# Kernel tuning notes

Measured on AMD Instinct MI355X. Metric: run time of the kernel, lower is better.

## Reference

```python
import jax, jax.numpy as jnp
import numpy as np

N_NODES = 100000


def _gcn_layer(x, src, dst, W, b, n_nodes):
    # x: [N, Cin]; src/dst already include self-loops
    h = x @ W  # [N, Cout]
    deg = jax.ops.segment_sum(jnp.ones_like(dst, dtype=h.dtype), dst,
                              num_segments=n_nodes)  # in-degree incl. self-loop
    dinv = jnp.where(deg > 0, deg ** -0.5, 0.0)
    norm = dinv[src] * dinv[dst]  # [E]
    msg = h[src] * norm[:, None]  # [E, Cout]
    out = jax.ops.segment_sum(msg, dst, num_segments=n_nodes)
    return out + b


def setup_inputs() -> dict:
    key = jax.random.key(0)
    k1, k2, k3, k4, k5, k6, k7 = jax.random.split(key, 7)
    E = 6400000
    x = jax.random.normal(k1, (N_NODES, 5), dtype=jnp.float32)
    edge_index = jax.random.randint(k2, (2, E), 0, N_NODES, dtype=jnp.int64)
    edge_f = jax.random.normal(k3, (E,), dtype=jnp.float32)
    edge_attr = jax.random.normal(k4, (E, 1), dtype=jnp.float32)
    # GCNConv params (glorot-ish scale)
    W1 = jax.random.normal(k5, (5, 8), dtype=jnp.float32) * (1.0 / np.sqrt(5))
    b1 = jnp.zeros((8,), dtype=jnp.float32)
    W2 = jax.random.normal(k6, (8, 5), dtype=jnp.float32) * (1.0 / np.sqrt(8))
    b2 = jnp.zeros((5,), dtype=jnp.float32)
    return {"x": x, "edge_index": edge_index, "edge_f": edge_f,
            "edge_attr": edge_attr, "W1": W1, "b1": b1, "W2": W2, "b2": b2}


def reference(x, edge_index, edge_f, edge_attr, W1, b1, W2, b2):
    n = x.shape[0]
    loops = jnp.arange(n, dtype=edge_index.dtype)
    src = jnp.concatenate([edge_index[0], loops])  # add self-loops (PyG default)
    dst = jnp.concatenate([edge_index[1], loops])
    h = _gcn_layer(x, src, dst, W1, b1, n)
    h = _gcn_layer(h, src, dst, W2, b2, n)
    return h
```

## Files before the change

kernel.cpp:

```cpp
#include <hip/hip_runtime.h>
#include <hip/hip_fp16.h>


#define TPB 256
#define VPB 256
#define B_BITS 8
#define MAXB 512
#define CAP 17408
#define NBLK_E 512
#define EPB 12500
#define SCT 512
#define DGT 512

typedef int int4e __attribute__((ext_vector_type(4)));
typedef _Float16 h8 __attribute__((ext_vector_type(8)));

__device__ __forceinline__ int4e ntload4(const int* p) {
    return __builtin_nontemporal_load((const int4e*)p);
}
__device__ __forceinline__ int ntload(const int* p) {
    return __builtin_nontemporal_load(p);
}

__global__ void k_init(int B, int* __restrict__ bpos) {
    int b = blockIdx.x * blockDim.x + threadIdx.x;
    if (b < B) bpos[b] = b * CAP;
}

__global__ __launch_bounds__(SCT) void k_scat(const int* __restrict__ src,
        const int* __restrict__ dst, int E, int B,
        int* __restrict__ bpos, int* __restrict__ pairs) {
    __shared__ int sorted[EPB];
    __shared__ int hist[MAXB], scn[MAXB], cur[MAXB], gbase[MAXB];
    int t = threadIdx.x;
    for (int i = t; i < MAXB; i += SCT) hist[i] = 0;
    __syncthreads();
    int lo = blockIdx.x * EPB;
    int n = min(E - lo, EPB);
    int n4 = n & ~3;
    for (int i = t * 4; i < n4; i += SCT * 4) {
        int4e d4 = ntload4(dst + lo + i);
        atomicAdd(&hist[d4.x >> B_BITS], 1);
        atomicAdd(&hist[d4.y >> B_BITS], 1);
        atomicAdd(&hist[d4.z >> B_BITS], 1);
        atomicAdd(&hist[d4.w >> B_BITS], 1);
    }
    for (int i = n4 + t; i < n; i += SCT)
        atomicAdd(&hist[dst[lo + i] >> B_BITS], 1);
    __syncthreads();
    if (t < MAXB) scn[t] = hist[t];
    __syncthreads();
    for (int off = 1; off < MAXB; off <<= 1) {
        int v = (t >= off && t < MAXB) ? scn[t - off] : 0;
        __syncthreads();
        if (t < MAXB) scn[t] += v;
        __syncthreads();
    }
    if (t < MAXB) {
        int h = hist[t];
        cur[t] = scn[t] - h;
        gbase[t] = (t < B && h) ? atomicAdd(&bpos[t], h) : 0;
    }
    __syncthreads();
    for (int i = t * 4; i < n4; i += SCT * 4) {
        int4e d4 = ntload4(dst + lo + i);
        int4e s4 = ntload4(src + lo + i);
        int p;
        p = atomicAdd(&cur[d4.x >> B_BITS], 1); sorted[p] = (s4.x << B_BITS) | (d4.x & (VPB - 1));
        p = atomicAdd(&cur[d4.y >> B_BITS], 1); sorted[p] = (s4.y << B_BITS) | (d4.y & (VPB - 1));
        p = atomicAdd(&cur[d4.z >> B_BITS], 1); sorted[p] = (s4.z << B_BITS) | (d4.z & (VPB - 1));
        p = atomicAdd(&cur[d4.w >> B_BITS], 1); sorted[p] = (s4.w << B_BITS) | (d4.w & (VPB - 1));
    }
    for (int i = n4 + t; i < n; i += SCT) {
        int d = dst[lo + i], s = src[lo + i];
        int p = atomicAdd(&cur[d >> B_BITS], 1);
        sorted[p] = (s << B_BITS) | (d & (VPB - 1));
    }
    __syncthreads();
    int wave = t >> 6, lane = t & 63;
    for (int b2 = wave; b2 < B; b2 += (SCT >> 6)) {
        int h = hist[b2];
        int st = scn[b2] - h;
        int gb = gbase[b2];
        for (int j = lane; j < h; j += 64)
            pairs[gb + j] = sorted[st + j];
    }
}

__global__ __launch_bounds__(DGT) void k_degxs(const int* __restrict__ pairs,
        const int* __restrict__ bpos, int N,
        const float* __restrict__ x,
        unsigned int* __restrict__ jinfo, _Float16* __restrict__ xs) {
    __shared__ int hist[VPB];
    __shared__ int scn[VPB];
    int t = threadIdx.x, b = blockIdx.x;
    if (t < VPB) hist[t] = 0;
    __syncthreads();
    int base = b * CAP;
    int n = bpos[b] - base, n4 = n & ~3;
    for (int i = t * 4; i < n4; i += DGT * 4) {
        int4e p = ntload4(pairs + base + i);
        atomicAdd(&hist[p.x & (VPB - 1)], 1);
        atomicAdd(&hist[p.y & (VPB - 1)], 1);
        atomicAdd(&hist[p.z & (VPB - 1)], 1);
        atomicAdd(&hist[p.w & (VPB - 1)], 1);
    }
    for (int i = n4 + t; i < n; i += DGT)
        atomicAdd(&hist[pairs[base + i] & (VPB - 1)], 1);
    __syncthreads();
    if (t < VPB) scn[t] = hist[t];
    __syncthreads();
    for (int off = 1; off < VPB; off <<= 1) {
        int v = (t >= off && t < VPB) ? scn[t - off] : 0;
        __syncthreads();
        if (t < VPB) scn[t] += v;
        __syncthreads();
    }
    int node = b * VPB + t;
    if (t < VPB && node < N) {
        int h = hist[t];
        int start = base + scn[t] - h;
        jinfo[node] = ((unsigned int)start << 9) | (unsigned int)h;
        float di = rsqrtf((float)(h + 1));
        const float* xp = x + (size_t)node * 5;
        h8 v;
        v[0] = (_Float16)(xp[0] * di); v[1] = (_Float16)(xp[1] * di);
        v[2] = (_Float16)(xp[2] * di); v[3] = (_Float16)(xp[3] * di);
        v[4] = (_Float16)(xp[4] * di);
        v[5] = (_Float16)0.f; v[6] = (_Float16)0.f; v[7] = (_Float16)0.f;
        *(h8*)(xs + (size_t)node * 8) = v;
    }
}

__global__ __launch_bounds__(1024) void k_agg1(const int* __restrict__ pairs_,
        const int* __restrict__ bpos, const unsigned int* __restrict__ jinfo,
        const _Float16* __restrict__ xs, const float* __restrict__ b1,
        const float* __restrict__ W1, const float* __restrict__ W2,
        _Float16* __restrict__ h2s, int N) {
    __shared__ int csr[CAP];
    __shared__ int js[VPB], ct[VPB], cur[VPB];
    int* pairs = (int*)pairs_;
    int t = threadIdx.x, b = blockIdx.x;
    int base = b * CAP;
    if (t < VPB) {
        int node = b * VPB + t;
        int s = 0, c = 0;
        if (node < N) {
            unsigned int u = jinfo[node];
            s = (int)(u >> 9) - base;
            c = (int)(u & 511u);
        }
        js[t] = s; ct[t] = c; cur[t] = s;
    }
    __syncthreads();
    int n = bpos[b] - base, n4 = n & ~3;
    for (int i = t * 4; i < n4; i += 1024 * 4) {
        int4e p = ntload4(pairs + base + i);
        int q;
        q = atomicAdd(&cur[p.x & (VPB - 1)], 1); csr[q] = p.x >> B_BITS;
        q = atomicAdd(&cur[p.y & (VPB - 1)], 1); csr[q] = p.y >> B_BITS;
        q = atomicAdd(&cur[p.z & (VPB - 1)], 1); csr[q] = p.z >> B_BITS;
        q = atomicAdd(&cur[p.w & (VPB - 1)], 1); csr[q] = p.w >> B_BITS;
    }
    for (int i = n4 + t; i < n; i += 1024) {
        int p = pairs[base + i];
        int q = atomicAdd(&cur[p & (VPB - 1)], 1);
        csr[q] = p >> B_BITS;
    }
    __syncthreads();
    for (int i = t; i < n; i += 1024)
        __builtin_nontemporal_store(csr[i], pairs + base + i);
    int lane = t & 3, ln = t >> 2;
    int node = b * VPB + ln;
    if (node >= N) return;
    int s0 = js[ln], cn = ct[ln];
    float a0 = 0.f, a1 = 0.f, a2 = 0.f, a3 = 0.f, a4 = 0.f;
    int j = lane;
    for (; j + 12 < cn; j += 16) {
        int sA = csr[s0 + j];
        int sB = csr[s0 + j + 4];
        int sC = csr[s0 + j + 8];
        int sD = csr[s0 + j + 12];
        h8 vA = *(const h8*)(xs + (size_t)sA * 8);
        h8 vB = *(const h8*)(xs + (size_t)sB * 8);
        h8 vC = *(const h8*)(xs + (size_t)sC * 8);
        h8 vD = *(const h8*)(xs + (size_t)sD * 8);
        a0 += (float)vA[0] + (float)vB[0] + (float)vC[0] + (float)vD[0];
        a1 += (float)vA[1] + (float)vB[1] + (float)vC[1] + (float)vD[1];
        a2 += (float)vA[2] + (float)vB[2] + (float)vC[2] + (float)vD[2];
        a3 += (float)vA[3] + (float)vB[3] + (float)vC[3] + (float)vD[3];
        a4 += (float)vA[4] + (float)vB[4] + (float)vC[4] + (float)vD[4];
    }
    for (; j < cn; j += 4) {
        int sA = csr[s0 + j];
        h8 vA = *(const h8*)(xs + (size_t)sA * 8);
        a0 += (float)vA[0]; a1 += (float)vA[1]; a2 += (float)vA[2];
        a3 += (float)vA[3]; a4 += (float)vA[4];
    }
#pragma unroll
    for (int d = 1; d < 4; d <<= 1) {
        a0 += __shfl_xor(a0, d); a1 += __shfl_xor(a1, d);
        a2 += __shfl_xor(a2, d); a3 += __shfl_xor(a3, d);
        a4 += __shfl_xor(a4, d);
    }
    h8 sv = *(const h8*)(xs + (size_t)node * 8);
    float tc[5];
    tc[0] = a0 + (float)sv[0]; tc[1] = a1 + (float)sv[1];
    tc[2] = a2 + (float)sv[2]; tc[3] = a3 + (float)sv[3];
    tc[4] = a4 + (float)sv[4];
    float di = rsqrtf((float)(cn + 1));
    float o1[8];
#pragma unroll
    for (int jj = 0; jj < 8; ++jj) {
        float h = 0.f;
#pragma unroll
        for (int c = 0; c < 5; ++c) h += tc[c] * W1[c * 8 + jj];
        o1[jj] = h * di + b1[jj];
    }
    if (lane == 0) {
        float hv[5];
#pragma unroll
        for (int k = 0; k < 5; ++k) {
            float h = 0.f;
#pragma unroll
            for (int jj = 0; jj < 8; ++jj) h += o1[jj] * W2[jj * 5 + k];
            hv[k] = h * di;
        }
        h8 w;
        w[0] = (_Float16)hv[0]; w[1] = (_Float16)hv[1]; w[2] = (_Float16)hv[2];
        w[3] = (_Float16)hv[3]; w[4] = (_Float16)hv[4];
        w[5] = (_Float16)0.f; w[6] = (_Float16)0.f; w[7] = (_Float16)0.f;
        *(h8*)(h2s + (size_t)node * 8) = w;
    }
}

__global__ __launch_bounds__(TPB) void k_agg2(const int* __restrict__ pairs,
        const unsigned int* __restrict__ jinfo, const _Float16* __restrict__ h2s,
        const float* __restrict__ b2, float* __restrict__ out, int N) {
    int gid = blockIdx.x * blockDim.x + threadIdx.x;
    int node = gid >> 3, lane = gid & 7;
    if (node >= N) return;
    unsigned int u = jinfo[node];
    int jsa = (int)(u >> 9), cn = (int)(u & 511u);
    float a0 = 0.f, a1 = 0.f, a2 = 0.f, a3 = 0.f, a4 = 0.f;
    int j = lane;
    for (; j + 24 < cn; j += 32) {
        int sA = ntload(pairs + jsa + j);
        int sB = ntload(pairs + jsa + j + 8);
        int sC = ntload(pairs + jsa + j + 16);
        int sD = ntload(pairs + jsa + j + 24);
        h8 vA = *(const h8*)(h2s + (size_t)sA * 8);
        h8 vB = *(const h8*)(h2s + (size_t)sB * 8);
        h8 vC = *(const h8*)(h2s + (size_t)sC * 8);
        h8 vD = *(const h8*)(h2s + (size_t)sD * 8);
        a0 += (float)vA[0] + (float)vB[0] + (float)vC[0] + (float)vD[0];
        a1 += (float)vA[1] + (float)vB[1] + (float)vC[1] + (float)vD[1];
        a2 += (float)vA[2] + (float)vB[2] + (float)vC[2] + (float)vD[2];
        a3 += (float)vA[3] + (float)vB[3] + (float)vC[3] + (float)vD[3];
        a4 += (float)vA[4] + (float)vB[4] + (float)vC[4] + (float)vD[4];
    }
    for (; j < cn; j += 8) {
        int sA = ntload(pairs + jsa + j);
        h8 vA = *(const h8*)(h2s + (size_t)sA * 8);
        a0 += (float)vA[0]; a1 += (float)vA[1]; a2 += (float)vA[2];
        a3 += (float)vA[3]; a4 += (float)vA[4];
    }
#pragma unroll
    for (int d = 1; d < 8; d <<= 1) {
        a0 += __shfl_xor(a0, d); a1 += __shfl_xor(a1, d);
        a2 += __shfl_xor(a2, d); a3 += __shfl_xor(a3, d);
        a4 += __shfl_xor(a4, d);
    }
    if (lane == 0) {
        float di = rsqrtf((float)(cn + 1));
        h8 sv = *(const h8*)(h2s + (size_t)node * 8);
        float* op = out + (size_t)node * 5;
        op[0] = (a0 + (float)sv[0]) * di + b2[0];
        op[1] = (a1 + (float)sv[1]) * di + b2[1];
        op[2] = (a2 + (float)sv[2]) * di + b2[2];
        op[3] = (a3 + (float)sv[3]) * di + b2[3];
        op[4] = (a4 + (float)sv[4]) * di + b2[4];
    }
}

extern "C" void kernel_launch(void* const* d_in, const int* in_sizes, int n_in,
                              void* d_out, int out_size, void* d_ws, size_t ws_size,
                              hipStream_t stream) {
    const float* x   = (const float*)d_in[0];
    const int*  eidx = (const int*)d_in[1];
    const float* W1 = (const float*)d_in[4];
    const float* b1 = (const float*)d_in[5];
    const float* W2 = (const float*)d_in[6];
    const float* b2 = (const float*)d_in[7];
    float* out = (float*)d_out;

    const int N = in_sizes[0] / 5;
    const int E = in_sizes[1] / 2;
    const int* src = eidx;
    const int* dst = eidx + E;

    const int B = (N + VPB - 1) / VPB;

    int*      pairs = (int*)d_ws;
    _Float16* xs    = (_Float16*)(pairs + (size_t)B * CAP);
    _Float16* h2s   = xs + (size_t)8 * N;
    unsigned int* jinfo = (unsigned int*)(h2s + (size_t)8 * N);
    int*      bpos  = (int*)(jinfo + N);

    const int g8N = (8 * N + TPB - 1) / TPB;

    k_init <<<(B + TPB - 1) / TPB, TPB, 0, stream>>>(B, bpos);
    k_scat <<<NBLK_E, SCT, 0, stream>>>(src, dst, E, B, bpos, pairs);
    k_degxs<<<B, DGT, 0, stream>>>(pairs, bpos, N, x, jinfo, xs);
    k_agg1 <<<B, 1024, 0, stream>>>(pairs, bpos, jinfo, xs, b1, W1, W2, h2s, N);
    k_agg2 <<<g8N, TPB, 0, stream>>>(pairs, jinfo, h2s, b2, out, N);
}
```

Baseline: 243.8 us.

## Halve bucket size to 128 nodes and vectorize layer-2 index loads

Shrinks each destination bucket from 256 to 128 nodes, which doubles the bucket count and cuts per-bucket capacity. That makes the aggregation kernel's shared CSR smaller, so it runs 512 threads per block and more blocks can fit per CU. The scatter kernel's prefix scan now handles two buckets per thread to cover 1024 buckets. The layer-2 gather reads four contiguous neighbor indices per lane with one unaligned vector load instead of four strided scalar loads. In exchange, a smaller CAP raises the risk of bucket overflow, and the unaligned vector loads may split across cache lines.

```diff
diff --git a/kernel.cpp b/kernel.cpp
--- a/kernel.cpp
+++ b/kernel.cpp
@@ -3,23 +3,22 @@
 
 
 #define TPB 256
-#define VPB 256
-#define B_BITS 8
-#define MAXB 512
-#define CAP 17408
+#define VPB 128
+#define B_BITS 7
+#define MAXB 1024
+#define CAP 9216
 #define NBLK_E 512
 #define EPB 12500
 #define SCT 512
 #define DGT 512
+#define AGT 512
 
 typedef int int4e __attribute__((ext_vector_type(4)));
+typedef int int4u __attribute__((ext_vector_type(4), aligned(4)));
 typedef _Float16 h8 __attribute__((ext_vector_type(8)));
 
 __device__ __forceinline__ int4e ntload4(const int* p) {
     return __builtin_nontemporal_load((const int4e*)p);
-}
-__device__ __forceinline__ int ntload(const int* p) {
-    return __builtin_nontemporal_load(p);
 }
 
 __global__ void k_init(int B, int* __restrict__ bpos) {
@@ -31,7 +30,8 @@
         const int* __restrict__ dst, int E, int B,
         int* __restrict__ bpos, int* __restrict__ pairs) {
     __shared__ int sorted[EPB];
-    __shared__ int hist[MAXB], scn[MAXB], cur[MAXB], gbase[MAXB];
+    __shared__ int hist[MAXB], cur[MAXB], gbase[MAXB];
+    __shared__ int scn[SCT];
     int t = threadIdx.x;
     for (int i = t; i < MAXB; i += SCT) hist[i] = 0;
     __syncthreads();
@@ -48,18 +48,22 @@
     for (int i = n4 + t; i < n; i += SCT)
         atomicAdd(&hist[dst[lo + i] >> B_BITS], 1);
     __syncthreads();
-    if (t < MAXB) scn[t] = hist[t];
-    __syncthreads();
-    for (int off = 1; off < MAXB; off <<= 1) {
-        int v = (t >= off && t < MAXB) ? scn[t - off] : 0;
+    int v0 = hist[2 * t], v1 = hist[2 * t + 1];
+    scn[t] = v0 + v1;
+    __syncthreads();
+    for (int off = 1; off < SCT; off <<= 1) {
+        int v = (t >= off) ? scn[t - off] : 0;
         __syncthreads();
-        if (t < MAXB) scn[t] += v;
+        scn[t] += v;
         __syncthreads();
     }
-    if (t < MAXB) {
-        int h = hist[t];
-        cur[t] = scn[t] - h;
-        gbase[t] = (t < B && h) ? atomicAdd(&bpos[t], h) : 0;
+    {
+        int excl = scn[t] - (v0 + v1);
+        cur[2 * t]     = excl;
+        cur[2 * t + 1] = excl + v0;
+        int b0 = 2 * t, b1 = 2 * t + 1;
+        gbase[b0] = (b0 < B && v0) ? atomicAdd(&bpos[b0], v0) : 0;
+        gbase[b1] = (b1 < B && v1) ? atomicAdd(&bpos[b1], v1) : 0;
     }
     __syncthreads();
     for (int i = t * 4; i < n4; i += SCT * 4) {
@@ -80,7 +84,7 @@
     int wave = t >> 6, lane = t & 63;
     for (int b2 = wave; b2 < B; b2 += (SCT >> 6)) {
         int h = hist[b2];
-        int st = scn[b2] - h;
+        int st = cur[b2] - h;
         int gb = gbase[b2];
         for (int j = lane; j < h; j += 64)
             pairs[gb + j] = sorted[st + j];
@@ -132,7 +136,7 @@
     }
 }
 
-__global__ __launch_bounds__(1024) void k_agg1(const int* __restrict__ pairs_,
+__global__ __launch_bounds__(AGT) void k_agg1(const int* __restrict__ pairs_,
         const int* __restrict__ bpos, const unsigned int* __restrict__ jinfo,
         const _Float16* __restrict__ xs, const float* __restrict__ b1,
         const float* __restrict__ W1, const float* __restrict__ W2,
@@ -154,7 +158,7 @@
     }
     __syncthreads();
     int n = bpos[b] - base, n4 = n & ~3;
-    for (int i = t * 4; i < n4; i += 1024 * 4) {
+    for (int i = t * 4; i < n4; i += AGT * 4) {
         int4e p = ntload4(pairs + base + i);
         int q;
         q = atomicAdd(&cur[p.x & (VPB - 1)], 1); csr[q] = p.x >> B_BITS;
@@ -162,13 +166,13 @@
         q = atomicAdd(&cur[p.z & (VPB - 1)], 1); csr[q] = p.z >> B_BITS;
         q = atomicAdd(&cur[p.w & (VPB - 1)], 1); csr[q] = p.w >> B_BITS;
     }
-    for (int i = n4 + t; i < n; i += 1024) {
+    for (int i = n4 + t; i < n; i += AGT) {
         int p = pairs[base + i];
         int q = atomicAdd(&cur[p & (VPB - 1)], 1);
         csr[q] = p >> B_BITS;
     }
     __syncthreads();
-    for (int i = t; i < n; i += 1024)
+    for (int i = t; i < n; i += AGT)
         __builtin_nontemporal_store(csr[i], pairs + base + i);
     int lane = t & 3, ln = t >> 2;
     int node = b * VPB + ln;
@@ -243,24 +247,22 @@
     unsigned int u = jinfo[node];
     int jsa = (int)(u >> 9), cn = (int)(u & 511u);
     float a0 = 0.f, a1 = 0.f, a2 = 0.f, a3 = 0.f, a4 = 0.f;
-    int j = lane;
-    for (; j + 24 < cn; j += 32) {
-        int sA = ntload(pairs + jsa + j);
-        int sB = ntload(pairs + jsa + j + 8);
-        int sC = ntload(pairs + jsa + j + 16);
-        int sD = ntload(pairs + jsa + j + 24);
-        h8 vA = *(const h8*)(h2s + (size_t)sA * 8);
-        h8 vB = *(const h8*)(h2s + (size_t)sB * 8);
-        h8 vC = *(const h8*)(h2s + (size_t)sC * 8);
-        h8 vD = *(const h8*)(h2s + (size_t)sD * 8);
+    int tiles = cn >> 5;
+    for (int it = 0; it < tiles; ++it) {
+        const int* cp = pairs + jsa + it * 32 + lane * 4;
+        int4u c4 = *(const int4u*)cp;
+        h8 vA = *(const h8*)(h2s + (size_t)c4.x * 8);
+        h8 vB = *(const h8*)(h2s + (size_t)c4.y * 8);
+        h8 vC = *(const h8*)(h2s + (size_t)c4.z * 8);
+        h8 vD = *(const h8*)(h2s + (size_t)c4.w * 8);
         a0 += (float)vA[0] + (float)vB[0] + (float)vC[0] + (float)vD[0];
         a1 += (float)vA[1] + (float)vB[1] + (float)vC[1] + (float)vD[1];
         a2 += (float)vA[2] + (float)vB[2] + (float)vC[2] + (float)vD[2];
         a3 += (float)vA[3] + (float)vB[3] + (float)vC[3] + (float)vD[3];
         a4 += (float)vA[4] + (float)vB[4] + (float)vC[4] + (float)vD[4];
     }
-    for (; j < cn; j += 8) {
-        int sA = ntload(pairs + jsa + j);
+    for (int j = tiles * 32 + lane; j < cn; j += 8) {
+        int sA = pairs[jsa + j];
         h8 vA = *(const h8*)(h2s + (size_t)sA * 8);
         a0 += (float)vA[0]; a1 += (float)vA[1]; a2 += (float)vA[2];
         a3 += (float)vA[3]; a4 += (float)vA[4];
@@ -312,6 +314,6 @@
     k_init <<<(B + TPB - 1) / TPB, TPB, 0, stream>>>(B, bpos);
     k_scat <<<NBLK_E, SCT, 0, stream>>>(src, dst, E, B, bpos, pairs);
     k_degxs<<<B, DGT, 0, stream>>>(pairs, bpos, N, x, jinfo, xs);
-    k_agg1 <<<B, 1024, 0, stream>>>(pairs, bpos, jinfo, xs, b1, W1, W2, h2s, N);
+    k_agg1 <<<B, AGT, 0, stream>>>(pairs, bpos, jinfo, xs, b1, W1, W2, h2s, N);
     k_agg2 <<<g8N, TPB, 0, stream>>>(pairs, jinfo, h2s, b2, out, N);
 }
```

After: 253.6 us. +4.0%, slower.
